# Optimization experiments

Hardware: AMD Instinct MI355X
Metric: run time of the kernel (lower is better)

Reference implementation:

```python
import jax, jax.numpy as jnp
import numpy as np

N = 50000      # nodes
E = 400000     # edges per hop
IN = 256       # in_channels
H = 4          # heads
C = 64         # out_channels per head
NEG = 0.2      # leaky relu negative slope


def setup_inputs() -> dict:
    key = jax.random.key(0)
    ks = jax.random.split(key, 10)
    x = jax.random.normal(ks[0], (N, IN), dtype=jnp.float32)
    edge_index1 = jax.random.randint(ks[1], (2, E), 0, N, dtype=jnp.int32)
    edge_index2 = jax.random.randint(ks[2], (2, E), 0, N, dtype=jnp.int32)
    s = 0.05
    Wl0 = jax.random.normal(ks[3], (IN, H * C), dtype=jnp.float32) * s
    Wr0 = jax.random.normal(ks[4], (IN, H * C), dtype=jnp.float32) * s
    att0 = jax.random.normal(ks[5], (H, C), dtype=jnp.float32) * s
    Wl1 = jax.random.normal(ks[6], (IN, H * C), dtype=jnp.float32) * s
    Wr1 = jax.random.normal(ks[7], (IN, H * C), dtype=jnp.float32) * s
    att1 = jax.random.normal(ks[8], (H, C), dtype=jnp.float32) * s
    return {"x": x, "Wl0": Wl0, "Wr0": Wr0, "att0": att0,
            "Wl1": Wl1, "Wr1": Wr1, "att1": att1,
            "edge_index1": edge_index1, "edge_index2": edge_index2}


def _gatv2_hop(x, Wl, Wr, att, src, dst):
    """One GATv2Conv hop (bias=False, residual=False, eval-mode dropout, concat=False)."""
    n = x.shape[0]
    xl = (x @ Wl).reshape(n, H, C)   # source-side projection
    xr = (x @ Wr).reshape(n, H, C)   # target-side projection
    # edge-wise GATv2 score: a^T leaky_relu(x_l[j] + x_r[i])
    m = jax.nn.leaky_relu(xl[src] + xr[dst], NEG)            # [E, H, C]
    e = jnp.einsum('ehc,hc->eh', m, att)                     # [E, H]
    # segment softmax over incoming edges of each destination node
    e_max = jax.lax.stop_gradient(
        jax.ops.segment_max(e, dst, num_segments=n))         # [N, H]
    ex = jnp.exp(e - e_max[dst])
    denom = jax.ops.segment_sum(ex, dst, num_segments=n)     # [N, H]
    alpha = ex / (denom[dst] + 1e-16)                        # [E, H]
    msg = xl[src] * alpha[:, :, None]                        # [E, H, C]
    out = jax.ops.segment_sum(msg, dst, num_segments=n)      # [N, H, C]
    return out.mean(axis=1)                                  # concat=False -> mean heads


def reference(x, Wl0, Wr0, att0, Wl1, Wr1, att1, edge_index1, edge_index2):
    n = x.shape[0]
    # hop 0: add_self_loops=True
    loop = jnp.arange(n, dtype=edge_index1.dtype)
    src0 = jnp.concatenate([edge_index1[0], loop])
    dst0 = jnp.concatenate([edge_index1[1], loop])
    out = _gatv2_hop(x, Wl0, Wr0, att0, src0, dst0)
    # hop 1: no self loops, scaled by 1/(k+1) = 1/2
    out = out + _gatv2_hop(x, Wl1, Wr1, att1, edge_index2[0], edge_index2[1]) / 2.0
    return out
```

## Files before the change

### kernel.cpp

```cpp
#include <hip/hip_runtime.h>

typedef unsigned int uint;
typedef unsigned short ushort;

typedef __bf16 bf16x8 __attribute__((ext_vector_type(8)));
typedef float f32x4 __attribute__((ext_vector_type(4)));
typedef float f32x2 __attribute__((ext_vector_type(2)));

#define CAP 48
#define RSTR 136

__device__ __forceinline__ ushort f2bf(float f) {
    uint u = __float_as_uint(f);
    u += 0x7fffu + ((u >> 16) & 1u);
    return (ushort)(u >> 16);
}
__device__ __forceinline__ void load_lds16(const ushort* g, ushort* l) {
    __builtin_amdgcn_global_load_lds(
        (const __attribute__((address_space(1))) void*)g,
        (__attribute__((address_space(3))) void*)l, 16, 0, 0);
}
__device__ __forceinline__ f32x2 up2(uint u) {
    f32x2 r;
    r.x = __uint_as_float(u << 16);
    r.y = __uint_as_float(u & 0xffff0000u);
    return r;
}

template<int CTRL>
__device__ __forceinline__ float dppadd(float p) {
    int t = __builtin_amdgcn_update_dpp(0, __float_as_int(p), CTRL, 0xf, 0xf, true);
    return p + __int_as_float(t);
}

__global__ __launch_bounds__(256) void prep_scatter(
    const float* __restrict__ X, ushort* __restrict__ Xb, int Nrows, int Mpad,
    const float* __restrict__ Wl0, const float* __restrict__ Wr0,
    const float* __restrict__ Wl1, const float* __restrict__ Wr1,
    ushort* __restrict__ Wt,
    const int* __restrict__ ei1, const int* __restrict__ ei2,
    int* __restrict__ cnt0, int* __restrict__ srcs0,
    int* __restrict__ cnt1, int* __restrict__ srcs1,
    int E1, int E2, int SB)
{
    int blk = blockIdx.x;
    if (blk < SB) {
        int e = blk * 256 + threadIdx.x;
        if (e < E1) {
            int d = ei1[E1 + e];
            int pos = atomicAdd(&cnt0[d], 1);
            if (pos < CAP) srcs0[(size_t)d * CAP + pos] = ei1[e];
        } else if (e < E1 + E2) {
            int e2 = e - E1;
            int d = ei2[E2 + e2];
            int pos = atomicAdd(&cnt1[d], 1);
            if (pos < CAP) srcs1[(size_t)d * CAP + pos] = ei2[e2];
        }
        return;
    }
    blk -= SB;
    const int BX = Mpad / 8;
    if (blk < BX) {
        int i = blk * 256 + threadIdx.x;
        int base = i * 8;
        int row = base >> 8;
        ushort o[8];
        if (row < Nrows) {
            float4 v0 = *(const float4*)(X + base);
            float4 v1 = *(const float4*)(X + base + 4);
            o[0] = f2bf(v0.x); o[1] = f2bf(v0.y); o[2] = f2bf(v0.z); o[3] = f2bf(v0.w);
            o[4] = f2bf(v1.x); o[5] = f2bf(v1.y); o[6] = f2bf(v1.z); o[7] = f2bf(v1.w);
        } else {
#pragma unroll
            for (int j = 0; j < 8; j++) o[j] = 0;
        }
        *(uint4*)(Xb + base) = *(const uint4*)o;
        return;
    }
    blk -= BX;
    int n = blk;
    int k = threadIdx.x;
    const float* W = (n < 256) ? Wl0 : (n < 512) ? Wr0 : (n < 768) ? Wl1 : Wr1;
    Wt[n * 256 + k] = f2bf(W[k * 256 + (n & 255)]);
}

__global__ __launch_bounds__(256, 2) void gemm_mfma(
    const ushort* __restrict__ Xb,
    const ushort* __restrict__ Wt,
    ushort* __restrict__ XP,
    int Nrows, int Pp, int nbshift)
{
    int b = blockIdx.x;
    int xcd = b & 7;
    int i = b >> 3;
    int p = xcd * Pp + (i >> nbshift);
    int j = i & ((1 << nbshift) - 1);
    const int m0 = p * 128;
    const int n0g = j * 128;

    __shared__ ushort SH[4 * 128 * 64];

    const int tid = threadIdx.x;
    const int w = tid >> 6, l = tid & 63;
    const int wm = w & 1, wn = w >> 1;

    f32x4 acc[4][4];
#pragma unroll
    for (int ii = 0; ii < 4; ii++)
#pragma unroll
        for (int jj = 0; jj < 4; jj++) acc[ii][jj] = (f32x4)(0.f);

    const int fr = l & 15, fq = l >> 4;
    int a_off[2][4], b_off[2][4];
#pragma unroll
    for (int g = 0; g < 2; g++)
#pragma unroll
        for (int t = 0; t < 4; t++) {
            int c = g * 4 + fq;
            int rA = wm * 64 + t * 16 + fr;
            a_off[g][t] = (rA * 8 + ((c + rA) & 7)) * 8;
            int rB = wn * 64 + t * 16 + fr;
            b_off[g][t] = (rB * 8 + ((c + rB) & 7)) * 8;
        }

    int srow[4], schunk[4];
#pragma unroll
    for (int rnd = 0; rnd < 4; rnd++) {
        int slot = rnd * 256 + tid;
        srow[rnd] = slot >> 3;
        schunk[rnd] = ((slot & 7) - srow[rnd]) & 7;
    }

#pragma unroll
    for (int rnd = 0; rnd < 4; rnd++) {
        load_lds16(Xb + (size_t)(m0 + srow[rnd]) * 256 + schunk[rnd] * 8,
                   &SH[(rnd * 256 + w * 64) * 8]);
        load_lds16(Wt + (size_t)(n0g + srow[rnd]) * 256 + schunk[rnd] * 8,
                   &SH[8192 + (rnd * 256 + w * 64) * 8]);
    }
    __syncthreads();

    int cur = 0;
    for (int t = 0; t < 4; t++) {
        const ushort* As = SH + cur * 16384;
        const ushort* Bs = As + 8192;
        if (t < 3) {
            ushort* An = SH + (cur ^ 1) * 16384;
            ushort* Bn = An + 8192;
            const int k0n = (t + 1) * 64;
#pragma unroll
            for (int rnd = 0; rnd < 4; rnd++) {
                load_lds16(Xb + (size_t)(m0 + srow[rnd]) * 256 + k0n + schunk[rnd] * 8,
                           &An[(rnd * 256 + w * 64) * 8]);
                load_lds16(Wt + (size_t)(n0g + srow[rnd]) * 256 + k0n + schunk[rnd] * 8,
                           &Bn[(rnd * 256 + w * 64) * 8]);
            }
        }
#pragma unroll
        for (int g = 0; g < 2; g++) {
            bf16x8 a[4], bfr[4];
#pragma unroll
            for (int t4 = 0; t4 < 4; t4++) {
                a[t4]   = *(const bf16x8*)(As + a_off[g][t4]);
                bfr[t4] = *(const bf16x8*)(Bs + b_off[g][t4]);
            }
#pragma unroll
            for (int mi = 0; mi < 4; mi++)
#pragma unroll
                for (int ni = 0; ni < 4; ni++)
                    acc[mi][ni] = __builtin_amdgcn_mfma_f32_16x16x32_bf16(
                        a[mi], bfr[ni], acc[mi][ni], 0, 0, 0);
        }
        __syncthreads();
        cur ^= 1;
    }

    ushort* OUT = XP + (size_t)(n0g >> 8) * ((size_t)Nrows * 256);
    const int colbase = n0g & 255;
    const int cb = wn * 64 + fr;
#pragma unroll
    for (int r = 0; r < 2; r++) {
        __syncthreads();
#pragma unroll
        for (int mm = 0; mm < 2; mm++) {
            int mi = 2 * r + mm;
            int brb = (wm * 32 + mm * 16 + fq * 4) * RSTR + cb;
#pragma unroll
            for (int reg = 0; reg < 4; reg++)
#pragma unroll
                for (int ni = 0; ni < 4; ni++)
                    SH[brb + reg * RSTR + ni * 16] = f2bf(acc[mi][ni][reg]);
        }
        __syncthreads();
        int br = tid >> 2;
        int grow = m0 + (br >> 5) * 64 + (2 * r + ((br >> 4) & 1)) * 16 + (br & 15);
        bool ok = (grow < Nrows);
        int cc = (tid & 3) * 8;
#pragma unroll
        for (int q = 0; q < 4; q++) {
            uint4 v = *(const uint4*)(SH + br * RSTR + cc + q * 32);
            if (ok) *(uint4*)(OUT + (size_t)grow * 256 + colbase + cc + q * 32) = v;
        }
    }
}

__device__ __forceinline__ uint4 pair_load(const ushort* __restrict__ XL, int sv,
                                           int e, int cp, uint hl, uint sub16)
{
    int eA = (e     < cp) ? e     : cp;
    int eB = (e + 1 < cp) ? e + 1 : cp;
    uint sA = (uint)__builtin_amdgcn_readlane(sv, eA) * 512u;
    uint sB = (uint)__builtin_amdgcn_readlane(sv, eB) * 512u;
    uint off = sA + hl * (sB - sA) + sub16;
    return *(const uint4*)((const char*)XL + off);
}

__device__ __forceinline__ void eaccp(uint4 raw, int deadB, uint hl,
    const f32x2* __restrict__ xr2, const f32x2* __restrict__ av2,
    f32x2* __restrict__ acc, float& den)
{
    f32x2 xv[4];
    xv[0] = up2(raw.x);
    xv[1] = up2(raw.y);
    xv[2] = up2(raw.z);
    xv[3] = up2(raw.w);
    f32x2 p2 = (f32x2)(0.f);
#pragma unroll
    for (int k = 0; k < 4; k++) {
        f32x2 t = xv[k] + xr2[k];
        f32x2 u = t * 0.2f;
        t = __builtin_elementwise_max(t, u);
        p2 += t * av2[k];
    }
    float p = p2.x + p2.y;
    p = dppadd<0xB1>(p);
    p = dppadd<0x4E>(p);
    p = dppadd<0x141>(p);
    float pe = __expf(p);
    if (deadB & (int)hl) pe = 0.f;
    den += pe;
#pragma unroll
    for (int k = 0; k < 4; k++) acc[k] += xv[k] * pe;
}

__device__ __forceinline__ void gat_hop(
    const ushort* __restrict__ XL, const ushort* __restrict__ XR,
    const float* __restrict__ att, const int* __restrict__ cnt,
    const int* __restrict__ srcs, int self, int d, int lane,
    uint hl, uint sub, uint sub16,
    f32x2* __restrict__ acc, float& den)
{
    uint4 xrr = *(const uint4*)((const char*)XR + (uint)d * 512u + sub16);
    f32x2 xr2[4];
    xr2[0] = up2(xrr.x);
    xr2[1] = up2(xrr.y);
    xr2[2] = up2(xrr.z);
    xr2[3] = up2(xrr.w);
    float4 a0 = *(const float4*)(att + sub * 8);
    float4 a1 = *(const float4*)(att + sub * 8 + 4);
    f32x2 av2[4];
    av2[0].x = a0.x; av2[0].y = a0.y;
    av2[1].x = a0.z; av2[1].y = a0.w;
    av2[2].x = a1.x; av2[2].y = a1.y;
    av2[3].x = a1.z; av2[3].y = a1.w;

#pragma unroll
    for (int k = 0; k < 4; k++) acc[k] = (f32x2)(0.f);
    den = 0.f;

    int m = __builtin_amdgcn_readfirstlane(cnt[d]);
    if (m > CAP) m = CAP;
    const int mt = m + self;
    if (mt <= 0) return;

    int idx = lane - self;
    int mm1 = (m > 0) ? (m - 1) : 0;
    int slot = idx < 0 ? 0 : (idx > mm1 ? mm1 : idx);
    int sv = srcs[(size_t)d * CAP + slot];
    if (self && lane == 0) sv = d;

    const int cp = mt - 1;
    uint4 pf0 = pair_load(XL, sv, 0, cp, hl, sub16);
    uint4 pf1 = pair_load(XL, sv, 2, cp, hl, sub16);
    for (int i = 0; i < mt; i += 4) {
        uint4 c0 = pf0, c1 = pf1;
        pf0 = pair_load(XL, sv, i + 4, cp, hl, sub16);
        pf1 = pair_load(XL, sv, i + 6, cp, hl, sub16);
        eaccp(c0, (i + 1 >= mt) ? 1 : 0, hl, xr2, av2, acc, den);
        if (i + 2 < mt)
            eaccp(c1, (i + 3 >= mt) ? 1 : 0, hl, xr2, av2, acc, den);
    }
}

__global__ __launch_bounds__(256) void gat_fused(
    const ushort* __restrict__ XL0, const ushort* __restrict__ XR0,
    const float* __restrict__ att0,
    const int* __restrict__ cnt0, const int* __restrict__ srcs0,
    int self0, float scale0,
    const ushort* __restrict__ XL1, const ushort* __restrict__ XR1,
    const float* __restrict__ att1,
    const int* __restrict__ cnt1, const int* __restrict__ srcs1,
    float scale1,
    const float* __restrict__ base, float* __restrict__ outp, int N)
{
    int d = blockIdx.x * 4 + (threadIdx.x >> 6);
    if (d >= N) return;
    int lane = threadIdx.x & 63;
    uint hl = (uint)(lane >> 5);
    uint sub = (uint)(lane & 31);
    uint sub16 = sub * 16u;

    f32x2 acc0[4];
    float den0;
    gat_hop(XL0, XR0, att0, cnt0, srcs0, self0, d, lane, hl, sub, sub16, acc0, den0);

    float v[8];
    den0 += __shfl_xor(den0, 32);
    float s0 = scale0 / (den0 + 1e-16f);
    if (cnt1) {
        f32x2 acc1[4];
        float den1;
        gat_hop(XL1, XR1, att1, cnt1, srcs1, 0, d, lane, hl, sub, sub16, acc1, den1);
        den1 += __shfl_xor(den1, 32);
        float s1 = scale1 / (den1 + 1e-16f);
#pragma unroll
        for (int k = 0; k < 4; k++) {
            v[2 * k]     = acc0[k].x * s0 + acc1[k].x * s1;
            v[2 * k + 1] = acc0[k].y * s0 + acc1[k].y * s1;
        }
    } else {
#pragma unroll
        for (int k = 0; k < 4; k++) {
            v[2 * k]     = acc0[k].x * s0;
            v[2 * k + 1] = acc0[k].y * s0;
        }
    }
#pragma unroll
    for (int j = 0; j < 8; j++) {
        v[j] += __shfl_xor(v[j], 8);
        v[j] += __shfl_xor(v[j], 16);
        v[j] += __shfl_xor(v[j], 32);
    }
    if (lane < 8) {
        float* dst = outp + (size_t)d * 64 + lane * 8;
        float4 w0 = {v[0], v[1], v[2], v[3]};
        float4 w1 = {v[4], v[5], v[6], v[7]};
        if (base) {
            float4 b0 = *(const float4*)(base + (size_t)d * 64 + lane * 8);
            float4 b1 = *(const float4*)(base + (size_t)d * 64 + lane * 8 + 4);
            w0.x += b0.x; w0.y += b0.y; w0.z += b0.z; w0.w += b0.w;
            w1.x += b1.x; w1.y += b1.y; w1.z += b1.z; w1.w += b1.w;
        }
        *(float4*)dst = w0;
        *(float4*)(dst + 4) = w1;
    }
}

extern "C" void kernel_launch(void* const* d_in, const int* in_sizes, int n_in,
                              void* d_out, int out_size, void* d_ws, size_t ws_size,
                              hipStream_t stream)
{
    const float* x    = (const float*)d_in[0];
    const float* Wl0  = (const float*)d_in[1];
    const float* Wr0  = (const float*)d_in[2];
    const float* att0 = (const float*)d_in[3];
    const float* Wl1  = (const float*)d_in[4];
    const float* Wr1  = (const float*)d_in[5];
    const float* att1 = (const float*)d_in[6];
    const int* ei1 = (const int*)d_in[7];
    const int* ei2 = (const int*)d_in[8];

    const int N  = in_sizes[0] / 256;
    const int E1 = in_sizes[7] / 2;
    const int E2 = in_sizes[8] / 2;
    const int Mpad = ((N + 1023) / 1024) * 1024;
    const int P  = Mpad / 128;
    const int Pp = P / 8;
    const size_t NB = (size_t)N * 256;

    char* ws = (char*)d_ws;
    size_t off = 0;
    ushort* Xb  = (ushort*)(ws + off); off += (size_t)Mpad * 256 * sizeof(ushort);
    ushort* Wt  = (ushort*)(ws + off); off += (size_t)1024 * 256 * sizeof(ushort);
    int* cnt0   = (int*)(ws + off);    off += (size_t)N * sizeof(int);
    int* cnt1   = (int*)(ws + off);    off += (size_t)N * sizeof(int);
    int* srcs0  = (int*)(ws + off);    off += (size_t)N * CAP * sizeof(int);
    int* srcs1  = (int*)(ws + off);    off += (size_t)N * CAP * sizeof(int);
    ushort* XP  = (ushort*)(ws + off);
    size_t need_mega = off + 4 * NB * sizeof(ushort);
    const bool mega = (ws_size >= need_mega);
    float* outf = (float*)d_out;

    hipMemsetAsync(cnt0, 0, 2 * (size_t)N * sizeof(int), stream);

    const int BX = Mpad / 8;
    const int SB = (E1 + E2 + 255) / 256;
    prep_scatter<<<SB + BX + 1024, 256, 0, stream>>>(
        x, Xb, N, Mpad, Wl0, Wr0, Wl1, Wr1, Wt,
        ei1, ei2, cnt0, srcs0, cnt1, srcs1, E1, E2, SB);

    int aggblk = (N + 3) / 4;
    if (mega) {
        gemm_mfma<<<P * 8, 256, 0, stream>>>(Xb, Wt, XP, N, Pp, 3);
        gat_fused<<<aggblk, 256, 0, stream>>>(
            XP, XP + NB, att0, cnt0, srcs0, 1, 0.25f,
            XP + 2 * NB, XP + 3 * NB, att1, cnt1, srcs1, 0.125f,
            nullptr, outf, N);
    } else {
        gemm_mfma<<<P * 4, 256, 0, stream>>>(Xb, Wt, XP, N, Pp, 2);
        gat_fused<<<aggblk, 256, 0, stream>>>(
            XP, XP + NB, att0, cnt0, srcs0, 1, 0.25f,
            nullptr, nullptr, nullptr, nullptr, nullptr, 0.f,
            nullptr, outf, N);
        gemm_mfma<<<P * 4, 256, 0, stream>>>(Xb, Wt + 512 * 256, XP, N, Pp, 2);
        gat_fused<<<aggblk, 256, 0, stream>>>(
            XP, XP + NB, att1, cnt1, srcs1, 0, 0.125f,
            nullptr, nullptr, nullptr, nullptr, nullptr, 0.f,
            outf, outf, N);
    }
}
```

Before: 253.1 us.

## Hoist both hops' index and target loads, deepen edge prefetch to three pairs

Moves the per-destination loads for both hops (source index slots, counts and target-side projection rows) to the kernel start, so their latency overlaps instead of being serialized before each hop. The edge loop now keeps three pair loads in flight instead of two. Slot clamping no longer depends on the count, so it can read padding entries of the source list, which are only ever used as masked edges. The deeper prefetch costs more registers and may lower occupancy.

```diff
diff --git a/kernel.cpp b/kernel.cpp
--- a/kernel.cpp
+++ b/kernel.cpp
@@ -243,14 +243,16 @@
     for (int k = 0; k < 4; k++) acc[k] += xv[k] * pe;
 }
 
-__device__ __forceinline__ void gat_hop(
-    const ushort* __restrict__ XL, const ushort* __restrict__ XR,
-    const float* __restrict__ att, const int* __restrict__ cnt,
-    const int* __restrict__ srcs, int self, int d, int lane,
-    uint hl, uint sub, uint sub16,
+__device__ __forceinline__ void gat_hop_core(
+    const ushort* __restrict__ XL, const float* __restrict__ att,
+    int mt, int sv, uint4 xrr, uint hl, uint sub, uint sub16,
     f32x2* __restrict__ acc, float& den)
 {
-    uint4 xrr = *(const uint4*)((const char*)XR + (uint)d * 512u + sub16);
+#pragma unroll
+    for (int k = 0; k < 4; k++) acc[k] = (f32x2)(0.f);
+    den = 0.f;
+    if (mt <= 0) return;
+
     f32x2 xr2[4];
     xr2[0] = up2(xrr.x);
     xr2[1] = up2(xrr.y);
@@ -264,31 +266,20 @@
     av2[2].x = a1.x; av2[2].y = a1.y;
     av2[3].x = a1.z; av2[3].y = a1.w;
 
-#pragma unroll
-    for (int k = 0; k < 4; k++) acc[k] = (f32x2)(0.f);
-    den = 0.f;
-
-    int m = __builtin_amdgcn_readfirstlane(cnt[d]);
-    if (m > CAP) m = CAP;
-    const int mt = m + self;
-    if (mt <= 0) return;
-
-    int idx = lane - self;
-    int mm1 = (m > 0) ? (m - 1) : 0;
-    int slot = idx < 0 ? 0 : (idx > mm1 ? mm1 : idx);
-    int sv = srcs[(size_t)d * CAP + slot];
-    if (self && lane == 0) sv = d;
-
     const int cp = mt - 1;
     uint4 pf0 = pair_load(XL, sv, 0, cp, hl, sub16);
     uint4 pf1 = pair_load(XL, sv, 2, cp, hl, sub16);
-    for (int i = 0; i < mt; i += 4) {
-        uint4 c0 = pf0, c1 = pf1;
-        pf0 = pair_load(XL, sv, i + 4, cp, hl, sub16);
-        pf1 = pair_load(XL, sv, i + 6, cp, hl, sub16);
+    uint4 pf2 = pair_load(XL, sv, 4, cp, hl, sub16);
+    for (int i = 0; i < mt; i += 6) {
+        uint4 c0 = pf0, c1 = pf1, c2 = pf2;
+        pf0 = pair_load(XL, sv, i + 6,  cp, hl, sub16);
+        pf1 = pair_load(XL, sv, i + 8,  cp, hl, sub16);
+        pf2 = pair_load(XL, sv, i + 10, cp, hl, sub16);
         eaccp(c0, (i + 1 >= mt) ? 1 : 0, hl, xr2, av2, acc, den);
         if (i + 2 < mt)
             eaccp(c1, (i + 3 >= mt) ? 1 : 0, hl, xr2, av2, acc, den);
+        if (i + 4 < mt)
+            eaccp(c2, (i + 5 >= mt) ? 1 : 0, hl, xr2, av2, acc, den);
     }
 }
 
@@ -310,9 +301,29 @@
     uint sub = (uint)(lane & 31);
     uint sub16 = sub * 16u;
 
+    int idx0 = lane - self0;
+    idx0 = idx0 < 0 ? 0 : (idx0 > CAP - 1 ? CAP - 1 : idx0);
+    int sv0 = srcs0[(size_t)d * CAP + idx0];
+    int m0 = __builtin_amdgcn_readfirstlane(cnt0[d]);
+    uint4 xrr0 = *(const uint4*)((const char*)XR0 + (uint)d * 512u + sub16);
+
+    int sv1 = 0, m1 = 0;
+    uint4 xrr1 = {0, 0, 0, 0};
+    if (cnt1) {
+        int idx1 = lane > CAP - 1 ? CAP - 1 : lane;
+        sv1 = srcs1[(size_t)d * CAP + idx1];
+        m1 = __builtin_amdgcn_readfirstlane(cnt1[d]);
+        xrr1 = *(const uint4*)((const char*)XR1 + (uint)d * 512u + sub16);
+    }
+
+    if (m0 > CAP) m0 = CAP;
+    const int mt0 = m0 + self0;
+    if (self0 && lane == 0) sv0 = d;
+    if (m1 > CAP) m1 = CAP;
+
     f32x2 acc0[4];
     float den0;
-    gat_hop(XL0, XR0, att0, cnt0, srcs0, self0, d, lane, hl, sub, sub16, acc0, den0);
+    gat_hop_core(XL0, att0, mt0, sv0, xrr0, hl, sub, sub16, acc0, den0);
 
     float v[8];
     den0 += __shfl_xor(den0, 32);
@@ -320,7 +331,7 @@
     if (cnt1) {
         f32x2 acc1[4];
         float den1;
-        gat_hop(XL1, XR1, att1, cnt1, srcs1, 0, d, lane, hl, sub, sub16, acc1, den1);
+        gat_hop_core(XL1, att1, m1, sv1, xrr1, hl, sub, sub16, acc1, den1);
         den1 += __shfl_xor(den1, 32);
         float s1 = scale1 / (den1 + 1e-16f);
 #pragma unroll
```

Result: no change. 253.3 us (+0.1%).

## Move edge bucketing scatter from prep kernel into GEMM epilogue

Applied to the files above, without the earlier changes.

The atomic edge-to-destination bucketing moves out of the prep kernel and into the tail of the MFMA GEMM kernel. Each GEMM block handles a contiguous chunk of edges after writing its output tile. This lets the latency-bound atomic scatter overlap with compute-bound GEMM work on other blocks and shortens the prep launch. In exchange, every GEMM block gets a longer tail, and the GEMM's register and occupancy behaviour may change. The fallback path passes zero edges to the second GEMM.

```diff
diff --git a/kernel.cpp b/kernel.cpp
--- a/kernel.cpp
+++ b/kernel.cpp
@@ -33,33 +33,14 @@
     return p + __int_as_float(t);
 }
 
-__global__ __launch_bounds__(256) void prep_scatter(
+__global__ __launch_bounds__(256) void prep(
     const float* __restrict__ X, ushort* __restrict__ Xb, int Nrows, int Mpad,
     const float* __restrict__ Wl0, const float* __restrict__ Wr0,
     const float* __restrict__ Wl1, const float* __restrict__ Wr1,
-    ushort* __restrict__ Wt,
-    const int* __restrict__ ei1, const int* __restrict__ ei2,
-    int* __restrict__ cnt0, int* __restrict__ srcs0,
-    int* __restrict__ cnt1, int* __restrict__ srcs1,
-    int E1, int E2, int SB)
-{
+    ushort* __restrict__ Wt)
+{
+    const int BX = Mpad / 8;
     int blk = blockIdx.x;
-    if (blk < SB) {
-        int e = blk * 256 + threadIdx.x;
-        if (e < E1) {
-            int d = ei1[E1 + e];
-            int pos = atomicAdd(&cnt0[d], 1);
-            if (pos < CAP) srcs0[(size_t)d * CAP + pos] = ei1[e];
-        } else if (e < E1 + E2) {
-            int e2 = e - E1;
-            int d = ei2[E2 + e2];
-            int pos = atomicAdd(&cnt1[d], 1);
-            if (pos < CAP) srcs1[(size_t)d * CAP + pos] = ei2[e2];
-        }
-        return;
-    }
-    blk -= SB;
-    const int BX = Mpad / 8;
     if (blk < BX) {
         int i = blk * 256 + threadIdx.x;
         int base = i * 8;
@@ -88,7 +69,11 @@
     const ushort* __restrict__ Xb,
     const ushort* __restrict__ Wt,
     ushort* __restrict__ XP,
-    int Nrows, int Pp, int nbshift)
+    int Nrows, int Pp, int nbshift,
+    const int* __restrict__ ei1, const int* __restrict__ ei2,
+    int* __restrict__ cnt0, int* __restrict__ srcs0,
+    int* __restrict__ cnt1, int* __restrict__ srcs1,
+    int E1, int E2, int EPB)
 {
     int b = blockIdx.x;
     int xcd = b & 7;
@@ -200,6 +185,23 @@
         for (int q = 0; q < 4; q++) {
             uint4 v = *(const uint4*)(SH + br * RSTR + cc + q * 32);
             if (ok) *(uint4*)(OUT + (size_t)grow * 256 + colbase + cc + q * 32) = v;
+        }
+    }
+
+    int e0 = blockIdx.x * EPB;
+    int e1 = e0 + EPB;
+    int etot = E1 + E2;
+    if (e1 > etot) e1 = etot;
+    for (int e = e0 + tid; e < e1; e += 256) {
+        if (e < E1) {
+            int dd = ei1[E1 + e];
+            int pos = atomicAdd(&cnt0[dd], 1);
+            if (pos < CAP) srcs0[(size_t)dd * CAP + pos] = ei1[e];
+        } else {
+            int e2 = e - E1;
+            int dd = ei2[E2 + e2];
+            int pos = atomicAdd(&cnt1[dd], 1);
+            if (pos < CAP) srcs1[(size_t)dd * CAP + pos] = ei2[e2];
         }
     }
 }
@@ -394,25 +396,32 @@
     hipMemsetAsync(cnt0, 0, 2 * (size_t)N * sizeof(int), stream);
 
     const int BX = Mpad / 8;
-    const int SB = (E1 + E2 + 255) / 256;
-    prep_scatter<<<SB + BX + 1024, 256, 0, stream>>>(
-        x, Xb, N, Mpad, Wl0, Wr0, Wl1, Wr1, Wt,
-        ei1, ei2, cnt0, srcs0, cnt1, srcs1, E1, E2, SB);
+    prep<<<BX + 1024, 256, 0, stream>>>(x, Xb, N, Mpad, Wl0, Wr0, Wl1, Wr1, Wt);
 
     int aggblk = (N + 3) / 4;
     if (mega) {
-        gemm_mfma<<<P * 8, 256, 0, stream>>>(Xb, Wt, XP, N, Pp, 3);
+        int G = P * 8;
+        int EPB = (E1 + E2 + G - 1) / G;
+        gemm_mfma<<<G, 256, 0, stream>>>(Xb, Wt, XP, N, Pp, 3,
+                                         ei1, ei2, cnt0, srcs0, cnt1, srcs1,
+                                         E1, E2, EPB);
         gat_fused<<<aggblk, 256, 0, stream>>>(
             XP, XP + NB, att0, cnt0, srcs0, 1, 0.25f,
             XP + 2 * NB, XP + 3 * NB, att1, cnt1, srcs1, 0.125f,
             nullptr, outf, N);
     } else {
-        gemm_mfma<<<P * 4, 256, 0, stream>>>(Xb, Wt, XP, N, Pp, 2);
+        int G = P * 4;
+        int EPB = (E1 + E2 + G - 1) / G;
+        gemm_mfma<<<G, 256, 0, stream>>>(Xb, Wt, XP, N, Pp, 2,
+                                         ei1, ei2, cnt0, srcs0, cnt1, srcs1,
+                                         E1, E2, EPB);
         gat_fused<<<aggblk, 256, 0, stream>>>(
             XP, XP + NB, att0, cnt0, srcs0, 1, 0.25f,
             nullptr, nullptr, nullptr, nullptr, nullptr, 0.f,
             nullptr, outf, N);
-        gemm_mfma<<<P * 4, 256, 0, stream>>>(Xb, Wt + 512 * 256, XP, N, Pp, 2);
+        gemm_mfma<<<G, 256, 0, stream>>>(Xb, Wt + 512 * 256, XP, N, Pp, 2,
+                                         nullptr, nullptr, cnt0, srcs0, cnt1, srcs1,
+                                         0, 0, 0);
         gat_fused<<<aggblk, 256, 0, stream>>>(
             XP, XP + NB, att1, cnt1, srcs1, 0, 0.125f,
             nullptr, nullptr, nullptr, nullptr, nullptr, 0.f,
```

New measurement: 261.1 us. 1.03x slower.
